# Kernel optimization log

Hardware: AMD Instinct MI355X
Metric: run time of the kernel (lower is better)

## Reference

```python
import jax, jax.numpy as jnp
import numpy as np
from jax.ops import segment_sum

N_NODES = 500000
N_EDGES = 1000000
N_GRAPHS = 20000
F_IN = 78


def gcn_conv(x, W, b, src, dst, n):
    # PyG GCNConv: add self-loops, symmetric normalization D^-1/2 A D^-1/2
    h = x @ W  # [N, Fout]
    deg = segment_sum(jnp.ones(src.shape[0], x.dtype), dst, num_segments=n) + 1.0  # self-loop
    dinv = jax.lax.rsqrt(deg)  # [N]
    norm = dinv[src] * dinv[dst]  # [E]
    agg = segment_sum(h[src] * norm[:, None], dst, num_segments=n)  # neighbor messages
    agg = agg + h * (dinv * dinv)[:, None]  # self-loop message
    return agg + b


def global_mean_pool(x, batch, n_graphs):
    s = segment_sum(x, batch, num_segments=n_graphs)
    cnt = segment_sum(jnp.ones(x.shape[0], x.dtype), batch, num_segments=n_graphs)
    return s / jnp.maximum(cnt, 1.0)[:, None]


def setup_inputs() -> dict:
    key = jax.random.key(0)
    ks = jax.random.split(key, 16)
    x = jax.random.normal(ks[0], (N_NODES, F_IN), dtype=jnp.float32)
    edge_index = jax.random.randint(ks[1], (2, N_EDGES), 0, N_NODES, dtype=jnp.int32)
    batch = jnp.sort(jax.random.randint(ks[2], (N_NODES,), 0, N_GRAPHS, dtype=jnp.int32))

    def lin(k, fi, fo):
        s = 1.0 / np.sqrt(fi)
        kw, kb = jax.random.split(k)
        return (jax.random.uniform(kw, (fi, fo), jnp.float32, -s, s),
                jax.random.uniform(kb, (fo,), jnp.float32, -s, s))

    W1, b1 = lin(ks[3], F_IN, F_IN)
    W2, b2 = lin(ks[4], F_IN, F_IN * 2)
    W3, b3 = lin(ks[5], F_IN * 2, F_IN * 4)
    fW1, fb1 = lin(ks[6], F_IN * 4, 1024)
    fW2, fb2 = lin(ks[7], 1024, 128)
    return {"x": x, "edge_index": edge_index, "batch": batch,
            "W1": W1, "b1": b1, "W2": W2, "b2": b2, "W3": W3, "b3": b3,
            "fW1": fW1, "fb1": fb1, "fW2": fW2, "fb2": fb2}


def reference(x, edge_index, batch, W1, b1, W2, b2, W3, b3, fW1, fb1, fW2, fb2):
    src, dst = edge_index[0], edge_index[1]
    n = x.shape[0]
    h = jax.nn.relu(gcn_conv(x, W1, b1, src, dst, n))
    h = jax.nn.relu(gcn_conv(h, W2, b2, src, dst, n))
    h = jax.nn.relu(gcn_conv(h, W3, b3, src, dst, n))
    g = global_mean_pool(h, batch, N_GRAPHS)  # [G, 312]
    g = jax.nn.relu(g @ fW1 + fb1)  # dropout is identity at eval
    return g @ fW2 + fb2
```

## Files before the change

kernel.cpp:

```cpp
#include <hip/hip_runtime.h>
#include <hip/hip_fp16.h>

#define N_NODES 500000
#define N_EDGES 1000000
#define N_GRAPHS 20000

typedef _Float16 f16x8 __attribute__((ext_vector_type(8)));
typedef float f32x4 __attribute__((ext_vector_type(4)));

__global__ __launch_bounds__(256) void fill_u32(unsigned* p, unsigned v, int n) {
  int i = blockIdx.x * 256 + threadIdx.x;
  if (i < n) p[i] = v;
}

__global__ __launch_bounds__(256) void hist_dst(const int* __restrict__ dst, int* cnt, int e) {
  int i = blockIdx.x * 256 + threadIdx.x;
  if (i < e) atomicAdd(&cnt[dst[i]], 1);
}

__global__ __launch_bounds__(256) void scanA(const int* __restrict__ deg, int* __restrict__ loc,
                                             int* __restrict__ partials, int n) {
  __shared__ int ts[256];
  int b = blockIdx.x, t = threadIdx.x;
  int base = b * 1024 + t * 4;
  int v[4], s = 0;
#pragma unroll
  for (int j = 0; j < 4; ++j) {
    v[j] = (base + j < n) ? deg[base + j] : 0;
    s += v[j];
  }
  ts[t] = s;
  __syncthreads();
  for (int off = 1; off < 256; off <<= 1) {
    int x = (t >= off) ? ts[t - off] : 0;
    __syncthreads();
    ts[t] += x;
    __syncthreads();
  }
  if (t == 255) partials[b] = ts[255];
  int run = ts[t] - s;
#pragma unroll
  for (int j = 0; j < 4; ++j) {
    if (base + j < n) loc[base + j] = run;
    run += v[j];
  }
}

__global__ __launch_bounds__(512) void scanB(int* partials, int nb) {
  __shared__ int s[512];
  int t = threadIdx.x;
  s[t] = (t < nb) ? partials[t] : 0;
  __syncthreads();
  if (t == 0) {
    int run = 0;
    for (int i = 0; i < nb; ++i) { int v = s[i]; s[i] = run; run += v; }
  }
  __syncthreads();
  if (t < nb) partials[t] = s[t];
}

__global__ __launch_bounds__(256) void scanC(int* __restrict__ rowptr, const int* __restrict__ partials,
                                             int* __restrict__ cur, int n, int e) {
  int i = blockIdx.x * 256 + threadIdx.x;
  if (i < n) {
    int v = rowptr[i] + partials[i >> 10];
    rowptr[i] = v;
    cur[i] = v;
  }
  if (i == 0) rowptr[n] = e;
}

__global__ __launch_bounds__(256) void dinv_k(const int* __restrict__ rowptr, float* dinv, int n) {
  int i = blockIdx.x * 256 + threadIdx.x;
  if (i < n) dinv[i] = rsqrtf(1.0f + (float)(rowptr[i + 1] - rowptr[i]));
}

__global__ __launch_bounds__(256) void bucket(const int* __restrict__ src, const int* __restrict__ dst,
                                              int* __restrict__ cur, int* __restrict__ ssrc, int e) {
  int i = blockIdx.x * 256 + threadIdx.x;
  if (i < e) ssrc[atomicAdd(&cur[dst[i]], 1)] = src[i];
}

__global__ __launch_bounds__(256) void ell_build(const int* __restrict__ rowptr,
                                                 const int* __restrict__ ssrc,
                                                 int4* __restrict__ ell, int n) {
  int i = blockIdx.x * 256 + threadIdx.x;
  if (i >= n) return;
  int r0 = rowptr[i], r1 = rowptr[i + 1];
  int deg = r1 - r0;
  int4 e;
  e.x = deg;
  e.y = (deg > 0) ? ssrc[r0] : 0;
  e.z = (deg > 1) ? ssrc[r0 + 1] : 0;
  e.w = (deg > 2) ? ssrc[r0 + 2] : 0;
  ell[i] = e;
}

__global__ __launch_bounds__(256) void graph_starts(const int* __restrict__ batch,
                                                    int* __restrict__ gstart, int n) {
  int i = blockIdx.x * 256 + threadIdx.x;
  if (i < n) {
    int b = batch[i];
    int bp = (i == 0) ? -1 : batch[i - 1];
    for (int g = bp + 1; g <= b; ++g) gstart[g] = i;
  } else if (i == n) {
    int bl = batch[n - 1];
    for (int g = bl + 1; g <= N_GRAPHS; ++g) gstart[g] = n;
  }
}

template <int CW>
__global__ __launch_bounds__(256) void wt_conv(const float* __restrict__ W, _Float16* __restrict__ WT,
                                               int K, int Nout, int ldw, int KP, int total) {
  int i = blockIdx.x * 256 + threadIdx.x;
  if (i >= total) return;
  int c = i / KP, kp = i - c * KP;
  int k; bool valid;
  if (CW) { int blk = kp / CW, r = kp - blk * CW; k = blk * 78 + r; valid = (r < 78) && (k < K); }
  else { k = kp; valid = kp < K; }
  WT[i] = (valid && c < Nout) ? (_Float16)W[(size_t)k * ldw + c] : (_Float16)0.f;
}

__global__ __launch_bounds__(256) void xconv(const float* __restrict__ xin,
                                             const float* __restrict__ dinv,
                                             _Float16* __restrict__ Xh) {
  unsigned idx = blockIdx.x * 256u + threadIdx.x;
  if (idx >= (unsigned)N_NODES * 48u) return;
  unsigned n = idx / 48u, c2 = idx - n * 48u;
  __half2 h = __floats2half2_rn(0.f, 0.f);
  if (c2 < 39u) {
    float di = dinv[n];
    float2 v = *reinterpret_cast<const float2*>(xin + (size_t)n * 78 + 2 * c2);
    h = __floats2half2_rn(v.x * di, v.y * di);
  }
  *reinterpret_cast<__half2*>((__half*)Xh + (size_t)n * 96 + 2 * c2) = h;
}

template <int KP, int OUT_MODE, int BLDS, int PLANE>
__global__ __launch_bounds__(256) void gemm_direct(
    const _Float16* __restrict__ in, const _Float16* __restrict__ WT,
    void* __restrict__ outp, const float* __restrict__ rs, const float* __restrict__ bo,
    int M, int Nout, int LDO, size_t planeStride) {
  constexpr int NS = KP / 32;
  constexpr bool HOIST = (NS <= 5);
  constexpr bool TSTORE = (BLDS != 0) && (OUT_MODE != 2);
  constexpr int BS_BYTES = BLDS ? 5 * NS * 64 * 16 : 16;
  constexpr int SM_BYTES = TSTORE ? (BS_BYTES > 20480 ? BS_BYTES : 20480) : BS_BYTES;
  __shared__ __align__(16) char smem[SM_BYTES];
  _Float16* Bs = (_Float16*)smem;
  const int tid = threadIdx.x;
  const int lane = tid & 63;
  const int wid = tid >> 6;
  const int row0 = blockIdx.y * 128;
  const int col0 = PLANE ? 0 : blockIdx.x * 80;
  const _Float16* wt = WT + (size_t)(PLANE ? blockIdx.x * 78 : col0) * KP;
  const float* bop = PLANE ? bo + blockIdx.x * 78 : bo;
  _Float16* out16 = (_Float16*)outp + (PLANE ? (size_t)blockIdx.x * planeStride : 0);
  float* out32 = (float*)outp;
  const int koff = (lane >> 4) * 8;
  const int gr0 = row0 + wid * 32 + (lane & 15);
  const bool v0 = gr0 < M, v1 = (gr0 + 16) < M;
  const _Float16* a0 = in + (size_t)gr0 * KP + koff;
  const _Float16* a1 = a0 + (size_t)16 * KP;
  const _Float16* bp = wt + (size_t)(lane & 15) * KP + koff;

  const f16x8 zf = {0, 0, 0, 0, 0, 0, 0, 0};
  const f32x4 z4 = {0.f, 0.f, 0.f, 0.f};

  f16x8 A0[HOIST ? NS : 1], A1[HOIST ? NS : 1];
  if constexpr (HOIST) {
#pragma unroll
    for (int s = 0; s < NS; ++s) {
      A0[s] = v0 ? *reinterpret_cast<const f16x8*>(a0 + s * 32) : zf;
      A1[s] = v1 ? *reinterpret_cast<const f16x8*>(a1 + s * 32) : zf;
    }
    __builtin_amdgcn_sched_barrier(0);
  }

  if (BLDS) {
    for (int i = tid; i < 5 * NS * 64; i += 256) {
      int l = i & 63;
      int nf = (i >> 6) % 5;
      int s = i / 320;
      int r = nf * 16 + (l & 15);
      int k = s * 32 + ((l >> 4) << 3);
      *reinterpret_cast<uint4*>(&Bs[(size_t)i * 8]) =
          *reinterpret_cast<const uint4*>(wt + (size_t)r * KP + k);
    }
    __syncthreads();
  }

  f32x4 acc[2][5];
#pragma unroll
  for (int a = 0; a < 2; ++a)
#pragma unroll
    for (int b = 0; b < 5; ++b) acc[a][b] = z4;

  if constexpr (HOIST) {
#pragma unroll
    for (int s = 0; s < NS; ++s) {
      f16x8 bf[5];
#pragma unroll
      for (int nf = 0; nf < 5; ++nf) {
        if (BLDS)
          bf[nf] = *reinterpret_cast<const f16x8*>(&Bs[((size_t)(s * 5 + nf) * 64 + lane) * 8]);
        else
          bf[nf] = *reinterpret_cast<const f16x8*>(bp + (size_t)nf * 16 * KP + s * 32);
      }
#pragma unroll
      for (int nf = 0; nf < 5; ++nf) {
        acc[0][nf] = __builtin_amdgcn_mfma_f32_16x16x32_f16(A0[s], bf[nf], acc[0][nf], 0, 0, 0);
        acc[1][nf] = __builtin_amdgcn_mfma_f32_16x16x32_f16(A1[s], bf[nf], acc[1][nf], 0, 0, 0);
      }
    }
  } else {
#pragma unroll
    for (int s = 0; s < NS; ++s) {
      f16x8 af0 = v0 ? *reinterpret_cast<const f16x8*>(a0 + s * 32) : zf;
      f16x8 af1 = v1 ? *reinterpret_cast<const f16x8*>(a1 + s * 32) : zf;
      f16x8 bf[5];
#pragma unroll
      for (int nf = 0; nf < 5; ++nf) {
        if (BLDS)
          bf[nf] = *reinterpret_cast<const f16x8*>(&Bs[((size_t)(s * 5 + nf) * 64 + lane) * 8]);
        else
          bf[nf] = *reinterpret_cast<const f16x8*>(bp + (size_t)nf * 16 * KP + s * 32);
      }
#pragma unroll
      for (int nf = 0; nf < 5; ++nf) {
        acc[0][nf] = __builtin_amdgcn_mfma_f32_16x16x32_f16(af0, bf[nf], acc[0][nf], 0, 0, 0);
        acc[1][nf] = __builtin_amdgcn_mfma_f32_16x16x32_f16(af1, bf[nf], acc[1][nf], 0, 0, 0);
      }
    }
  }

  if constexpr (TSTORE) {
    __syncthreads();
    _Float16* Os = (_Float16*)smem;
#pragma unroll
    for (int rf = 0; rf < 2; ++rf) {
#pragma unroll
      for (int j = 0; j < 4; ++j) {
        int rl = wid * 32 + rf * 16 + (lane >> 4) * 4 + j;
        int gr = row0 + rl;
        float sc = (OUT_MODE == 3 && gr < M) ? rs[gr] : 0.f;
#pragma unroll
        for (int nf = 0; nf < 5; ++nf) {
          int cl = nf * 16 + (lane & 15);
          int oc = col0 + cl;
          float r = 0.f;
          if (oc < Nout) {
            r = fmaxf(acc[rf][nf][j] + bop[oc], 0.f);
            if (OUT_MODE == 3) r *= sc;
          }
          Os[rl * 80 + cl] = (_Float16)r;
        }
      }
    }
    __syncthreads();
    for (int i = tid; i < 1280; i += 256) {
      int rl = i / 10, u = i - rl * 10;
      int gr = row0 + rl;
      if (gr < M)
        *reinterpret_cast<uint4*>(&out16[(size_t)gr * LDO + col0 + u * 8]) =
            *reinterpret_cast<const uint4*>(&Os[rl * 80 + u * 8]);
    }
  } else {
#pragma unroll
    for (int rf = 0; rf < 2; ++rf) {
#pragma unroll
      for (int j = 0; j < 4; ++j) {
        int gr = row0 + wid * 32 + rf * 16 + (lane >> 4) * 4 + j;
        if (gr >= M) continue;
        float sc = (OUT_MODE == 3) ? rs[gr] : 0.f;
#pragma unroll
        for (int nf = 0; nf < 5; ++nf) {
          int oc = col0 + nf * 16 + (lane & 15);
          if (oc >= Nout) continue;
          float v = acc[rf][nf][j];
          if (OUT_MODE == 1) {
            out16[(size_t)gr * LDO + oc] = (_Float16)fmaxf(v + bop[oc], 0.f);
          } else if (OUT_MODE == 3) {
            out16[(size_t)gr * LDO + oc] = (_Float16)(fmaxf(v + bop[oc], 0.f) * sc);
          } else {
            out32[(size_t)gr * LDO + oc] = v + bop[oc];
          }
        }
      }
    }
  }
}

__device__ inline void acc8(float* a, uint4 v) {
  const __half2* h = reinterpret_cast<const __half2*>(&v);
#pragma unroll
  for (int j = 0; j < 4; ++j) {
    float2 f = __half22float2(h[j]);
    a[2 * j] += f.x;
    a[2 * j + 1] += f.y;
  }
}

template <int LDI>
__device__ inline void gather_sumT(float* a, const _Float16* hbase, unsigned n,
                                   const int4* __restrict__ ell,
                                   const int* __restrict__ rowptr,
                                   const int* __restrict__ ssrc) {
  int4 e = ell[n];
  const int deg = e.x;
  uint4 sv = *reinterpret_cast<const uint4*>(hbase + (size_t)n * LDI);
  uint4 g0, g1, g2;
  if (deg > 0) g0 = *reinterpret_cast<const uint4*>(hbase + (size_t)e.y * LDI);
  if (deg > 1) g1 = *reinterpret_cast<const uint4*>(hbase + (size_t)e.z * LDI);
  if (deg > 2) g2 = *reinterpret_cast<const uint4*>(hbase + (size_t)e.w * LDI);
  {
    const __half2* h = reinterpret_cast<const __half2*>(&sv);
#pragma unroll
    for (int j = 0; j < 4; ++j) {
      float2 f = __half22float2(h[j]);
      a[2 * j] = f.x;
      a[2 * j + 1] = f.y;
    }
  }
  if (deg > 0) acc8(a, g0);
  if (deg > 1) acc8(a, g1);
  if (deg > 2) acc8(a, g2);
  if (deg > 3) {
    int r = rowptr[n] + 3, r1 = r + deg - 3;
    for (; r + 2 <= r1; r += 2) {
      uint4 va = *reinterpret_cast<const uint4*>(hbase + (size_t)ssrc[r] * LDI);
      uint4 vb = *reinterpret_cast<const uint4*>(hbase + (size_t)ssrc[r + 1] * LDI);
      acc8(a, va);
      acc8(a, vb);
    }
    if (r < r1) {
      uint4 va = *reinterpret_cast<const uint4*>(hbase + (size_t)ssrc[r] * LDI);
      acc8(a, va);
    }
  }
}

template <int LDI, int NSUB>
__global__ __launch_bounds__(256) void aggregateZ(
    const _Float16* __restrict__ in, const int4* __restrict__ ell,
    const int* __restrict__ rowptr, const int* __restrict__ ssrc,
    const float* __restrict__ dinv, _Float16* __restrict__ outZ, int ldo) {
  unsigned idx = blockIdx.x * 256u + threadIdx.x;
  if (idx >= (unsigned)N_NODES * NSUB) return;
  unsigned n = idx / NSUB, sub = idx - n * NSUB;
  float a[8];
  gather_sumT<LDI>(a, in + sub * 8u, n, ell, rowptr, ssrc);
  float di = dinv[n];
  _Float16 ov[8];
#pragma unroll
  for (int j = 0; j < 8; ++j) ov[j] = (_Float16)(di * a[j]);
  *reinterpret_cast<uint4*>(outZ + (size_t)n * ldo + sub * 8u) =
      *reinterpret_cast<const uint4*>(ov);
}

__global__ __launch_bounds__(256) void pool_seq(
    const _Float16* __restrict__ in, const int* __restrict__ gstart,
    _Float16* __restrict__ GA, int inOff, int coffGA) {
  unsigned idx = blockIdx.x * 256u + threadIdx.x;
  if (idx >= (unsigned)N_GRAPHS * 10u) return;
  unsigned g = idx / 10u, q = idx - g * 10u;
  int n0 = gstart[g], n1 = gstart[g + 1];
  const _Float16* base = in + inOff + q * 8;
  float a[8] = {0.f, 0.f, 0.f, 0.f, 0.f, 0.f, 0.f, 0.f};
  float b2[8] = {0.f, 0.f, 0.f, 0.f, 0.f, 0.f, 0.f, 0.f};
  int n = n0;
  for (; n + 2 <= n1; n += 2) {
    uint4 va = *reinterpret_cast<const uint4*>(base + (size_t)n * 160);
    uint4 vb = *reinterpret_cast<const uint4*>(base + (size_t)(n + 1) * 160);
    acc8(a, va);
    acc8(b2, vb);
  }
  if (n < n1) {
    uint4 va = *reinterpret_cast<const uint4*>(base + (size_t)n * 160);
    acc8(a, va);
  }
  float gi = 1.0f / fmaxf((float)(n1 - n0), 1.0f);
  _Float16 ov[8];
#pragma unroll
  for (int j = 0; j < 8; ++j) ov[j] = (_Float16)((a[j] + b2[j]) * gi);
  *reinterpret_cast<uint4*>(GA + (size_t)g * 320 + coffGA + q * 8) =
      *reinterpret_cast<const uint4*>(ov);
}

extern "C" void kernel_launch(void* const* d_in, const int* in_sizes, int n_in,
                              void* d_out, int out_size, void* d_ws, size_t ws_size,
                              hipStream_t stream) {
  const float* x   = (const float*)d_in[0];
  const int* ei    = (const int*)d_in[1];
  const int* batch = (const int*)d_in[2];
  const float* W1 = (const float*)d_in[3];
  const float* b1 = (const float*)d_in[4];
  const float* W2 = (const float*)d_in[5];
  const float* b2 = (const float*)d_in[6];
  const float* W3 = (const float*)d_in[7];
  const float* b3 = (const float*)d_in[8];
  const float* fW1 = (const float*)d_in[9];
  const float* fb1 = (const float*)d_in[10];
  const float* fW2 = (const float*)d_in[11];
  const float* fb2 = (const float*)d_in[12];
  float* out = (float*)d_out;

  const int Nn = N_NODES, E = N_EDGES, G = N_GRAPHS;
  const int* src = ei;
  const int* dst = ei + E;

  _Float16* A = (_Float16*)d_ws;
  _Float16* B = A + (size_t)Nn * 160;
  _Float16* GA = B + (size_t)Nn * 160;
  _Float16* W1T   = GA + (size_t)G * 320;
  _Float16* W2T   = W1T + 80 * 96;
  _Float16* W3T   = W2T + 160 * 96;
  _Float16* fW1T  = W3T + 320 * 160;
  _Float16* fW2T  = fW1T + (size_t)1040 * 320;
  float* dinv     = (float*)(fW2T + (size_t)160 * 1056);
  int* rowptr     = (int*)(dinv + Nn);
  int* cur        = rowptr + Nn + 1;
  int* ssrc       = cur + Nn;
  int* partials   = ssrc + E;
  int* gstart     = partials + 512;
  int4* ell = (int4*)(((uintptr_t)(gstart + G + 1) + 15) & ~(uintptr_t)15);

  _Float16* Xh = A;
  _Float16* Z1 = B;
  _Float16* H1 = A;
  _Float16* Z2 = B;
  _Float16* H2 = A;
  _Float16* Z3 = B;
  _Float16* O3 = A;
  _Float16* fc1 = B;

  dim3 blk(256);
  const int gN10 = (int)(((unsigned)Nn * 10u + 255u) / 256u);
  const int gN20 = (int)(((unsigned)Nn * 20u + 255u) / 256u);
  const int gG10 = (int)(((unsigned)G * 10u + 255u) / 256u);
  const dim3 nodeGrid(1, (Nn + 127) / 128);
  const dim3 pairGrid(2, (Nn + 127) / 128);
  const int NB = (Nn + 1023) / 1024;

  fill_u32<<<(Nn + 255) / 256, blk, 0, stream>>>((unsigned*)cur, 0u, Nn);
  hist_dst<<<(E + 255) / 256, blk, 0, stream>>>(dst, cur, E);
  scanA<<<NB, blk, 0, stream>>>(cur, rowptr, partials, Nn);
  scanB<<<1, 512, 0, stream>>>(partials, NB);
  scanC<<<(Nn + 255) / 256, blk, 0, stream>>>(rowptr, partials, cur, Nn, E);
  dinv_k<<<(Nn + 255) / 256, blk, 0, stream>>>(rowptr, dinv, Nn);
  bucket<<<(E + 255) / 256, blk, 0, stream>>>(src, dst, cur, ssrc, E);
  ell_build<<<(Nn + 255) / 256, blk, 0, stream>>>(rowptr, ssrc, ell, Nn);
  graph_starts<<<(Nn + 256) / 256, blk, 0, stream>>>(batch, gstart, Nn);

  wt_conv<0><<<(80 * 96 + 255) / 256, blk, 0, stream>>>(W1, W1T, 78, 78, 78, 96, 80 * 96);
  wt_conv<0><<<(160 * 96 + 255) / 256, blk, 0, stream>>>(W2, W2T, 78, 156, 156, 96, 160 * 96);
  wt_conv<80><<<(320 * 160 + 255) / 256, blk, 0, stream>>>(W3, W3T, 156, 312, 312, 160, 320 * 160);
  wt_conv<80><<<(1040 * 320 + 255) / 256, blk, 0, stream>>>(fW1, fW1T, 312, 1024, 1024, 320, 1040 * 320);
  wt_conv<0><<<(160 * 1056 + 255) / 256, blk, 0, stream>>>(fW2, fW2T, 1024, 128, 128, 1056, 160 * 1056);

  xconv<<<(int)(((unsigned)Nn * 48u + 255u) / 256u), blk, 0, stream>>>(x, dinv, Xh);

  aggregateZ<96, 10><<<gN10, blk, 0, stream>>>(Xh, ell, rowptr, ssrc, dinv, Z1, 96);
  gemm_direct<96, 3, 1, 0><<<nodeGrid, blk, 0, stream>>>(Z1, W1T, H1, dinv, b1, Nn, 78, 96, 0);

  aggregateZ<96, 10><<<gN10, blk, 0, stream>>>(H1, ell, rowptr, ssrc, dinv, Z2, 96);
  gemm_direct<96, 3, 1, 1><<<pairGrid, blk, 0, stream>>>(Z2, W2T, H2, dinv, b2, Nn, 78, 160, 80);

  aggregateZ<160, 20><<<gN20, blk, 0, stream>>>(H2, ell, rowptr, ssrc, dinv, Z3, 160);
  for (int p = 0; p < 2; ++p) {
    gemm_direct<160, 1, 1, 1><<<pairGrid, blk, 0, stream>>>(
        Z3, W3T + (size_t)(156 * p) * 160, O3, nullptr, b3 + 156 * p, Nn, 78, 160, 80);
    pool_seq<<<gG10, blk, 0, stream>>>(O3, gstart, GA, 0, (2 * p) * 80);
    pool_seq<<<gG10, blk, 0, stream>>>(O3, gstart, GA, 80, (2 * p + 1) * 80);
  }

  {
    dim3 g((1024 + 79) / 80, (G + 127) / 128);
    gemm_direct<320, 1, 1, 0><<<g, blk, 0, stream>>>(GA, fW1T, fc1, nullptr, fb1, G, 1024, 1056, 0);
  }
  {
    dim3 g((128 + 79) / 80, (G + 127) / 128);
    gemm_direct<1056, 2, 0, 0><<<g, blk, 0, stream>>>(fc1, fW2T, out, nullptr, fb2, G, 128, 128, 0);
  }
}
```

Baseline: 1.020 ms.

## Add async-LDS GEMM for node layers with padded row strides

Adds a new gemm_lds kernel that uses global_load_lds to copy a 64-row A tile and the weight tile asynchronously into LDS, then runs MFMA from LDS. Node feature rows are padded (96→104, 160→168) so LDS row strides avoid bank conflicts, and the aggregation, pooling and weight-conversion kernels are updated to match. The node-level GEMMs switch to 64-row blocks, giving more blocks with smaller tiles. The cost is more memory traffic from the padding and the loss of the two-row-fragment register reuse of the old direct GEMM.

New measurement: 1.030 ms. No clear change (+0.9%).

```diff
diff --git a/kernel.cpp b/kernel.cpp
--- a/kernel.cpp
+++ b/kernel.cpp
@@ -111,13 +111,13 @@
 
 template <int CW>
 __global__ __launch_bounds__(256) void wt_conv(const float* __restrict__ W, _Float16* __restrict__ WT,
-                                               int K, int Nout, int ldw, int KP, int total) {
+                                               int K, int Nout, int ldw, int KPL, int STRIDE, int total) {
   int i = blockIdx.x * 256 + threadIdx.x;
   if (i >= total) return;
-  int c = i / KP, kp = i - c * KP;
-  int k; bool valid;
-  if (CW) { int blk = kp / CW, r = kp - blk * CW; k = blk * 78 + r; valid = (r < 78) && (k < K); }
-  else { k = kp; valid = kp < K; }
+  int c = i / STRIDE, kp = i - c * STRIDE;
+  int k = kp; bool valid = kp < KPL;
+  if (CW) { int blk = kp / CW, r = kp - blk * CW; k = blk * 78 + r; valid = valid && (r < 78) && (k < K); }
+  else { valid = valid && (kp < K); }
   WT[i] = (valid && c < Nout) ? (_Float16)W[(size_t)k * ldw + c] : (_Float16)0.f;
 }
 
@@ -125,24 +125,100 @@
                                              const float* __restrict__ dinv,
                                              _Float16* __restrict__ Xh) {
   unsigned idx = blockIdx.x * 256u + threadIdx.x;
-  if (idx >= (unsigned)N_NODES * 48u) return;
-  unsigned n = idx / 48u, c2 = idx - n * 48u;
+  if (idx >= (unsigned)N_NODES * 52u) return;
+  unsigned n = idx / 52u, c2 = idx - n * 52u;
   __half2 h = __floats2half2_rn(0.f, 0.f);
   if (c2 < 39u) {
     float di = dinv[n];
     float2 v = *reinterpret_cast<const float2*>(xin + (size_t)n * 78 + 2 * c2);
     h = __floats2half2_rn(v.x * di, v.y * di);
   }
-  *reinterpret_cast<__half2*>((__half*)Xh + (size_t)n * 96 + 2 * c2) = h;
-}
-
-template <int KP, int OUT_MODE, int BLDS, int PLANE>
+  *reinterpret_cast<__half2*>((__half*)Xh + (size_t)n * 104 + 2 * c2) = h;
+}
+
+__device__ __forceinline__ void async16(const void* g, void* l) {
+  __builtin_amdgcn_global_load_lds(
+      (const __attribute__((address_space(1))) void*)g,
+      (__attribute__((address_space(3))) void*)l, 16, 0, 0);
+}
+
+template <int KPL, int STRIDE, int OUT_MODE>
+__global__ __launch_bounds__(256) void gemm_lds(
+    const _Float16* __restrict__ in, const _Float16* __restrict__ WT,
+    _Float16* __restrict__ outp, const float* __restrict__ rs,
+    const float* __restrict__ bo, int M, int LDO) {
+  constexpr int NS = KPL / 32;
+  constexpr int SB = STRIDE * 2;
+  constexpr int CA = (64 * SB) / 1024;
+  constexpr int CB = (80 * SB + 1023) / 1024;
+  __shared__ __align__(16) _Float16 As[64 * STRIDE];
+  __shared__ __align__(16) _Float16 Bs[CB * 512];
+  const int tid = threadIdx.x;
+  const int lane = tid & 63;
+  const int wid = tid >> 6;
+  const int row0 = blockIdx.y * 64;
+  const _Float16* wt = WT + (size_t)(blockIdx.x * 78) * STRIDE;
+  _Float16* out = outp + (size_t)blockIdx.x * 80;
+  const float* bop = bo + blockIdx.x * 78;
+
+  const char* ab = (const char*)in + (size_t)row0 * SB;
+  for (int c = wid; c < CA; c += 4)
+    async16(ab + (size_t)c * 1024 + lane * 16, (char*)As + c * 1024);
+  const char* bb = (const char*)wt;
+  for (int c = wid; c < CB; c += 4)
+    async16(bb + (size_t)c * 1024 + lane * 16, (char*)Bs + c * 1024);
+  __syncthreads();
+
+  const int r16 = lane & 15, q = lane >> 4;
+  const f32x4 z4 = {0.f, 0.f, 0.f, 0.f};
+  f32x4 acc[5];
+#pragma unroll
+  for (int nf = 0; nf < 5; ++nf) acc[nf] = z4;
+
+#pragma unroll
+  for (int s = 0; s < NS; ++s) {
+    f16x8 af = *reinterpret_cast<const f16x8*>(&As[(wid * 16 + r16) * STRIDE + s * 32 + q * 8]);
+#pragma unroll
+    for (int nf = 0; nf < 5; ++nf) {
+      f16x8 bf = *reinterpret_cast<const f16x8*>(&Bs[(nf * 16 + r16) * STRIDE + s * 32 + q * 8]);
+      acc[nf] = __builtin_amdgcn_mfma_f32_16x16x32_f16(af, bf, acc[nf], 0, 0, 0);
+    }
+  }
+
+  __syncthreads();
+  _Float16* Os = As;
+#pragma unroll
+  for (int j = 0; j < 4; ++j) {
+    int rl = wid * 16 + q * 4 + j;
+    int gr = row0 + rl;
+    float sc = (OUT_MODE == 3 && gr < M) ? rs[gr] : 1.f;
+#pragma unroll
+    for (int nf = 0; nf < 5; ++nf) {
+      int cl = nf * 16 + r16;
+      float v = 0.f;
+      if (cl < 78) {
+        v = fmaxf(acc[nf][j] + bop[cl], 0.f);
+        if (OUT_MODE == 3) v *= sc;
+      }
+      Os[rl * 80 + cl] = (_Float16)v;
+    }
+  }
+  __syncthreads();
+  for (int i = tid; i < 640; i += 256) {
+    int rl = i / 10, u = i - rl * 10;
+    int gr = row0 + rl;
+    if (gr < M)
+      *reinterpret_cast<uint4*>(&out[(size_t)gr * LDO + u * 8]) =
+          *reinterpret_cast<const uint4*>(&Os[rl * 80 + u * 8]);
+  }
+}
+
+template <int KP, int OUT_MODE, int BLDS>
 __global__ __launch_bounds__(256) void gemm_direct(
     const _Float16* __restrict__ in, const _Float16* __restrict__ WT,
-    void* __restrict__ outp, const float* __restrict__ rs, const float* __restrict__ bo,
-    int M, int Nout, int LDO, size_t planeStride) {
+    void* __restrict__ outp, const float* __restrict__ bo,
+    int M, int Nout, int LDO) {
   constexpr int NS = KP / 32;
-  constexpr bool HOIST = (NS <= 5);
   constexpr bool TSTORE = (BLDS != 0) && (OUT_MODE != 2);
   constexpr int BS_BYTES = BLDS ? 5 * NS * 64 * 16 : 16;
   constexpr int SM_BYTES = TSTORE ? (BS_BYTES > 20480 ? BS_BYTES : 20480) : BS_BYTES;
@@ -152,10 +228,9 @@
   const int lane = tid & 63;
   const int wid = tid >> 6;
   const int row0 = blockIdx.y * 128;
-  const int col0 = PLANE ? 0 : blockIdx.x * 80;
-  const _Float16* wt = WT + (size_t)(PLANE ? blockIdx.x * 78 : col0) * KP;
-  const float* bop = PLANE ? bo + blockIdx.x * 78 : bo;
-  _Float16* out16 = (_Float16*)outp + (PLANE ? (size_t)blockIdx.x * planeStride : 0);
+  const int col0 = blockIdx.x * 80;
+  const _Float16* wt = WT + (size_t)col0 * KP;
+  _Float16* out16 = (_Float16*)outp;
   float* out32 = (float*)outp;
   const int koff = (lane >> 4) * 8;
   const int gr0 = row0 + wid * 32 + (lane & 15);
@@ -163,19 +238,6 @@
   const _Float16* a0 = in + (size_t)gr0 * KP + koff;
   const _Float16* a1 = a0 + (size_t)16 * KP;
   const _Float16* bp = wt + (size_t)(lane & 15) * KP + koff;
-
-  const f16x8 zf = {0, 0, 0, 0, 0, 0, 0, 0};
-  const f32x4 z4 = {0.f, 0.f, 0.f, 0.f};
-
-  f16x8 A0[HOIST ? NS : 1], A1[HOIST ? NS : 1];
-  if constexpr (HOIST) {
-#pragma unroll
-    for (int s = 0; s < NS; ++s) {
-      A0[s] = v0 ? *reinterpret_cast<const f16x8*>(a0 + s * 32) : zf;
-      A1[s] = v1 ? *reinterpret_cast<const f16x8*>(a1 + s * 32) : zf;
-    }
-    __builtin_amdgcn_sched_barrier(0);
-  }
 
   if (BLDS) {
     for (int i = tid; i < 5 * NS * 64; i += 256) {
@@ -190,47 +252,30 @@
     __syncthreads();
   }
 
+  const f16x8 zf = {0, 0, 0, 0, 0, 0, 0, 0};
+  const f32x4 z4 = {0.f, 0.f, 0.f, 0.f};
   f32x4 acc[2][5];
 #pragma unroll
   for (int a = 0; a < 2; ++a)
 #pragma unroll
     for (int b = 0; b < 5; ++b) acc[a][b] = z4;
 
-  if constexpr (HOIST) {
-#pragma unroll
-    for (int s = 0; s < NS; ++s) {
-      f16x8 bf[5];
-#pragma unroll
-      for (int nf = 0; nf < 5; ++nf) {
-        if (BLDS)
-          bf[nf] = *reinterpret_cast<const f16x8*>(&Bs[((size_t)(s * 5 + nf) * 64 + lane) * 8]);
-        else
-          bf[nf] = *reinterpret_cast<const f16x8*>(bp + (size_t)nf * 16 * KP + s * 32);
-      }
-#pragma unroll
-      for (int nf = 0; nf < 5; ++nf) {
-        acc[0][nf] = __builtin_amdgcn_mfma_f32_16x16x32_f16(A0[s], bf[nf], acc[0][nf], 0, 0, 0);
-        acc[1][nf] = __builtin_amdgcn_mfma_f32_16x16x32_f16(A1[s], bf[nf], acc[1][nf], 0, 0, 0);
-      }
-    }
-  } else {
-#pragma unroll
-    for (int s = 0; s < NS; ++s) {
-      f16x8 af0 = v0 ? *reinterpret_cast<const f16x8*>(a0 + s * 32) : zf;
-      f16x8 af1 = v1 ? *reinterpret_cast<const f16x8*>(a1 + s * 32) : zf;
-      f16x8 bf[5];
-#pragma unroll
-      for (int nf = 0; nf < 5; ++nf) {
-        if (BLDS)
-          bf[nf] = *reinterpret_cast<const f16x8*>(&Bs[((size_t)(s * 5 + nf) * 64 + lane) * 8]);
-        else
-          bf[nf] = *reinterpret_cast<const f16x8*>(bp + (size_t)nf * 16 * KP + s * 32);
-      }
-#pragma unroll
-      for (int nf = 0; nf < 5; ++nf) {
-        acc[0][nf] = __builtin_amdgcn_mfma_f32_16x16x32_f16(af0, bf[nf], acc[0][nf], 0, 0, 0);
-        acc[1][nf] = __builtin_amdgcn_mfma_f32_16x16x32_f16(af1, bf[nf], acc[1][nf], 0, 0, 0);
-      }
+#pragma unroll
+  for (int s = 0; s < NS; ++s) {
+    f16x8 af0 = v0 ? *reinterpret_cast<const f16x8*>(a0 + s * 32) : zf;
+    f16x8 af1 = v1 ? *reinterpret_cast<const f16x8*>(a1 + s * 32) : zf;
+    f16x8 bf[5];
+#pragma unroll
+    for (int nf = 0; nf < 5; ++nf) {
+      if (BLDS)
+        bf[nf] = *reinterpret_cast<const f16x8*>(&Bs[((size_t)(s * 5 + nf) * 64 + lane) * 8]);
+      else
+        bf[nf] = *reinterpret_cast<const f16x8*>(bp + (size_t)nf * 16 * KP + s * 32);
+    }
+#pragma unroll
+    for (int nf = 0; nf < 5; ++nf) {
+      acc[0][nf] = __builtin_amdgcn_mfma_f32_16x16x32_f16(af0, bf[nf], acc[0][nf], 0, 0, 0);
+      acc[1][nf] = __builtin_amdgcn_mfma_f32_16x16x32_f16(af1, bf[nf], acc[1][nf], 0, 0, 0);
     }
   }
 
@@ -242,17 +287,12 @@
 #pragma unroll
       for (int j = 0; j < 4; ++j) {
         int rl = wid * 32 + rf * 16 + (lane >> 4) * 4 + j;
-        int gr = row0 + rl;
-        float sc = (OUT_MODE == 3 && gr < M) ? rs[gr] : 0.f;
 #pragma unroll
         for (int nf = 0; nf < 5; ++nf) {
           int cl = nf * 16 + (lane & 15);
           int oc = col0 + cl;
           float r = 0.f;
-          if (oc < Nout) {
-            r = fmaxf(acc[rf][nf][j] + bop[oc], 0.f);
-            if (OUT_MODE == 3) r *= sc;
-          }
+          if (oc < Nout) r = fmaxf(acc[rf][nf][j] + bo[oc], 0.f);
           Os[rl * 80 + cl] = (_Float16)r;
         }
       }
@@ -272,19 +312,13 @@
       for (int j = 0; j < 4; ++j) {
         int gr = row0 + wid * 32 + rf * 16 + (lane >> 4) * 4 + j;
         if (gr >= M) continue;
-        float sc = (OUT_MODE == 3) ? rs[gr] : 0.f;
 #pragma unroll
         for (int nf = 0; nf < 5; ++nf) {
           int oc = col0 + nf * 16 + (lane & 15);
           if (oc >= Nout) continue;
           float v = acc[rf][nf][j];
-          if (OUT_MODE == 1) {
-            out16[(size_t)gr * LDO + oc] = (_Float16)fmaxf(v + bop[oc], 0.f);
-          } else if (OUT_MODE == 3) {
-            out16[(size_t)gr * LDO + oc] = (_Float16)(fmaxf(v + bop[oc], 0.f) * sc);
-          } else {
-            out32[(size_t)gr * LDO + oc] = v + bop[oc];
-          }
+          if (OUT_MODE == 1) out16[(size_t)gr * LDO + oc] = (_Float16)fmaxf(v + bo[oc], 0.f);
+          else out32[(size_t)gr * LDO + oc] = v + bo[oc];
         }
       }
     }
@@ -370,13 +404,13 @@
   float b2[8] = {0.f, 0.f, 0.f, 0.f, 0.f, 0.f, 0.f, 0.f};
   int n = n0;
   for (; n + 2 <= n1; n += 2) {
-    uint4 va = *reinterpret_cast<const uint4*>(base + (size_t)n * 160);
-    uint4 vb = *reinterpret_cast<const uint4*>(base + (size_t)(n + 1) * 160);
+    uint4 va = *reinterpret_cast<const uint4*>(base + (size_t)n * 168);
+    uint4 vb = *reinterpret_cast<const uint4*>(base + (size_t)(n + 1) * 168);
     acc8(a, va);
     acc8(b2, vb);
   }
   if (n < n1) {
-    uint4 va = *reinterpret_cast<const uint4*>(base + (size_t)n * 160);
+    uint4 va = *reinterpret_cast<const uint4*>(base + (size_t)n * 168);
     acc8(a, va);
   }
   float gi = 1.0f / fmaxf((float)(n1 - n0), 1.0f);
@@ -410,12 +444,12 @@
   const int* dst = ei + E;
 
   _Float16* A = (_Float16*)d_ws;
-  _Float16* B = A + (size_t)Nn * 160;
-  _Float16* GA = B + (size_t)Nn * 160;
+  _Float16* B = A + (size_t)Nn * 168;
+  _Float16* GA = B + (size_t)Nn * 168;
   _Float16* W1T   = GA + (size_t)G * 320;
-  _Float16* W2T   = W1T + 80 * 96;
-  _Float16* W3T   = W2T + 160 * 96;
-  _Float16* fW1T  = W3T + 320 * 160;
+  _Float16* W2T   = W1T + 96 * 104;
+  _Float16* W3T   = W2T + 160 * 104;
+  _Float16* fW1T  = W3T + 320 * 168;
   _Float16* fW2T  = fW1T + (size_t)1040 * 320;
   float* dinv     = (float*)(fW2T + (size_t)160 * 1056);
   int* rowptr     = (int*)(dinv + Nn);
@@ -435,11 +469,11 @@
   _Float16* fc1 = B;
 
   dim3 blk(256);
-  const int gN10 = (int)(((unsigned)Nn * 10u + 255u) / 256u);
+  const int gN13 = (int)(((unsigned)Nn * 13u + 255u) / 256u);
   const int gN20 = (int)(((unsigned)Nn * 20u + 255u) / 256u);
   const int gG10 = (int)(((unsigned)G * 10u + 255u) / 256u);
-  const dim3 nodeGrid(1, (Nn + 127) / 128);
-  const dim3 pairGrid(2, (Nn + 127) / 128);
+  const dim3 oneGrid(1, (Nn + 63) / 64);
+  const dim3 pairGrid(2, (Nn + 63) / 64);
   const int NB = (Nn + 1023) / 1024;
 
   fill_u32<<<(Nn + 255) / 256, blk, 0, stream>>>((unsigned*)cur, 0u, Nn);
@@ -452,34 +486,34 @@
   ell_build<<<(Nn + 255) / 256, blk, 0, stream>>>(rowptr, ssrc, ell, Nn);
   graph_starts<<<(Nn + 256) / 256, blk, 0, stream>>>(batch, gstart, Nn);
 
-  wt_conv<0><<<(80 * 96 + 255) / 256, blk, 0, stream>>>(W1, W1T, 78, 78, 78, 96, 80 * 96);
-  wt_conv<0><<<(160 * 96 + 255) / 256, blk, 0, stream>>>(W2, W2T, 78, 156, 156, 96, 160 * 96);
-  wt_conv<80><<<(320 * 160 + 255) / 256, blk, 0, stream>>>(W3, W3T, 156, 312, 312, 160, 320 * 160);
-  wt_conv<80><<<(1040 * 320 + 255) / 256, blk, 0, stream>>>(fW1, fW1T, 312, 1024, 1024, 320, 1040 * 320);
-  wt_conv<0><<<(160 * 1056 + 255) / 256, blk, 0, stream>>>(fW2, fW2T, 1024, 128, 128, 1056, 160 * 1056);
-
-  xconv<<<(int)(((unsigned)Nn * 48u + 255u) / 256u), blk, 0, stream>>>(x, dinv, Xh);
-
-  aggregateZ<96, 10><<<gN10, blk, 0, stream>>>(Xh, ell, rowptr, ssrc, dinv, Z1, 96);
-  gemm_direct<96, 3, 1, 0><<<nodeGrid, blk, 0, stream>>>(Z1, W1T, H1, dinv, b1, Nn, 78, 96, 0);
-
-  aggregateZ<96, 10><<<gN10, blk, 0, stream>>>(H1, ell, rowptr, ssrc, dinv, Z2, 96);
-  gemm_direct<96, 3, 1, 1><<<pairGrid, blk, 0, stream>>>(Z2, W2T, H2, dinv, b2, Nn, 78, 160, 80);
-
-  aggregateZ<160, 20><<<gN20, blk, 0, stream>>>(H2, ell, rowptr, ssrc, dinv, Z3, 160);
+  wt_conv<0><<<(96 * 104 + 255) / 256, blk, 0, stream>>>(W1, W1T, 78, 78, 78, 96, 104, 96 * 104);
+  wt_conv<0><<<(160 * 104 + 255) / 256, blk, 0, stream>>>(W2, W2T, 78, 156, 156, 96, 104, 160 * 104);
+  wt_conv<80><<<(320 * 168 + 255) / 256, blk, 0, stream>>>(W3, W3T, 156, 312, 312, 160, 168, 320 * 168);
+  wt_conv<80><<<(1040 * 320 + 255) / 256, blk, 0, stream>>>(fW1, fW1T, 312, 1024, 1024, 320, 320, 1040 * 320);
+  wt_conv<0><<<(160 * 1056 + 255) / 256, blk, 0, stream>>>(fW2, fW2T, 1024, 128, 128, 1056, 1056, 160 * 1056);
+
+  xconv<<<(int)(((unsigned)Nn * 52u + 255u) / 256u), blk, 0, stream>>>(x, dinv, Xh);
+
+  aggregateZ<104, 13><<<gN13, blk, 0, stream>>>(Xh, ell, rowptr, ssrc, dinv, Z1, 104);
+  gemm_lds<96, 104, 3><<<oneGrid, blk, 0, stream>>>(Z1, W1T, H1, dinv, b1, Nn, 104);
+
+  aggregateZ<104, 13><<<gN13, blk, 0, stream>>>(H1, ell, rowptr, ssrc, dinv, Z2, 104);
+  gemm_lds<96, 104, 3><<<pairGrid, blk, 0, stream>>>(Z2, W2T, H2, dinv, b2, Nn, 168);
+
+  aggregateZ<168, 20><<<gN20, blk, 0, stream>>>(H2, ell, rowptr, ssrc, dinv, Z3, 168);
   for (int p = 0; p < 2; ++p) {
-    gemm_direct<160, 1, 1, 1><<<pairGrid, blk, 0, stream>>>(
-        Z3, W3T + (size_t)(156 * p) * 160, O3, nullptr, b3 + 156 * p, Nn, 78, 160, 80);
+    gemm_lds<160, 168, 1><<<pairGrid, blk, 0, stream>>>(
+        Z3, W3T + (size_t)(156 * p) * 168, O3, nullptr, b3 + 156 * p, Nn, 168);
     pool_seq<<<gG10, blk, 0, stream>>>(O3, gstart, GA, 0, (2 * p) * 80);
     pool_seq<<<gG10, blk, 0, stream>>>(O3, gstart, GA, 80, (2 * p + 1) * 80);
   }
 
   {
     dim3 g((1024 + 79) / 80, (G + 127) / 128);
-    gemm_direct<320, 1, 1, 0><<<g, blk, 0, stream>>>(GA, fW1T, fc1, nullptr, fb1, G, 1024, 1056, 0);
+    gemm_direct<320, 1, 1><<<g, blk, 0, stream>>>(GA, fW1T, fc1, fb1, G, 1024, 1056);
   }
   {
     dim3 g((128 + 79) / 80, (G + 127) / 128);
-    gemm_direct<1056, 2, 0, 0><<<g, blk, 0, stream>>>(fc1, fW2T, out, nullptr, fb2, G, 128, 128, 0);
-  }
-}
+    gemm_direct<1056, 2, 0><<<g, blk, 0, stream>>>(fc1, fW2T, out, fb2, G, 128, 128);
+  }
+}
```
